# Optimization experiments

Hardware: AMD Instinct MI355X
Metric: run time of the kernel (lower is better)

## Reference

```python
import jax, jax.numpy as jnp
import numpy as np

NUM_HEADS = 16
EMB_SIZE = 1024
HEAD_SIZE = 64


def setup_inputs() -> dict:
    key = jax.random.key(0)
    ks = jax.random.split(key, 9)
    H, E, D = NUM_HEADS, EMB_SIZE, HEAD_SIZE
    s = 1.0 / np.sqrt(E)
    X = jax.random.normal(ks[0], (4, 2048, E), dtype=jnp.float32)
    Wq = jax.random.uniform(ks[1], (H, E, D), jnp.float32, -s, s)
    Wk = jax.random.uniform(ks[2], (H, E, D), jnp.float32, -s, s)
    Wv = jax.random.uniform(ks[3], (H, E, D), jnp.float32, -s, s)
    bq = jax.random.uniform(ks[4], (H, D), jnp.float32, -s, s)
    bk = jax.random.uniform(ks[5], (H, D), jnp.float32, -s, s)
    bv = jax.random.uniform(ks[6], (H, D), jnp.float32, -s, s)
    so = 1.0 / np.sqrt(H * D)
    Wo = jax.random.uniform(ks[7], (H * D, E), jnp.float32, -so, so)
    bo = jax.random.uniform(ks[8], (E,), jnp.float32, -so, so)
    return {"X": X, "Wq": Wq, "Wk": Wk, "Wv": Wv, "bq": bq, "bk": bk, "bv": bv, "Wo": Wo, "bo": bo}


def reference(X, Wq, Wk, Wv, bq, bk, bv, Wo, bo):
    B, S, E = X.shape
    H, _, D = Wq.shape
    # per-head projections (batched over heads)
    q = jnp.einsum('bse,hed->bhsd', X, Wq) + bq[None, :, None, :]
    k = jnp.einsum('bse,hed->bhsd', X, Wk) + bk[None, :, None, :]
    v = jnp.einsum('bse,hed->bhsd', X, Wv) + bv[None, :, None, :]
    # causal scaled-dot-product attention
    scores = jnp.einsum('bhsd,bhtd->bhst', q, k) / jnp.sqrt(jnp.float32(D))
    causal = jnp.tril(jnp.ones((S, S), dtype=bool))
    scores = jnp.where(causal[None, None], scores, jnp.float32(-jnp.inf))
    probs = jax.nn.softmax(scores, axis=-1)
    out = jnp.einsum('bhst,bhtd->bhsd', probs, v)
    # concat heads (head h occupies slots [h*D:(h+1)*D]) then output proj
    concat = out.transpose(0, 2, 1, 3).reshape(B, S, H * D)
    # dropout is identity in eval mode
    return concat @ Wo + bo
```

## Files before the change

### kernel.cpp

```cpp
#include <hip/hip_runtime.h>
#include <stdint.h>


typedef float   f32x4  __attribute__((ext_vector_type(4)));
typedef __bf16  bf16x8 __attribute__((ext_vector_type(8)));
typedef short   short8 __attribute__((ext_vector_type(8)));
typedef unsigned short ushort4v __attribute__((ext_vector_type(4)));

typedef __attribute__((address_space(1))) void GV;
typedef __attribute__((address_space(3))) void LV;

#define DEVI static __device__ __forceinline__

DEVI unsigned short f2bf(float f){
  unsigned u = __float_as_uint(f);
  unsigned r = u + 0x7fffu + ((u>>16)&1u);
  return (unsigned short)(r>>16);
}

DEVI unsigned cvt_pk_bf16(float lo, float hi){
  unsigned r;
  asm("v_cvt_pk_bf16_f32 %0, %1, %2" : "=v"(r) : "v"(lo), "v"(hi));
  return r;
}

DEVI void permlane32_swap(unsigned &a, unsigned &b){
  asm volatile("v_permlane32_swap_b32 %0, %1" : "+v"(a), "+v"(b));
}
DEVI void permlane16_swap(unsigned &a, unsigned &b){
  asm volatile("v_permlane16_swap_b32 %0, %1" : "+v"(a), "+v"(b));
}

DEVI void gl_lds16(const void* g, void* l){
  __builtin_amdgcn_global_load_lds((GV*)g, (LV*)l, 16, 0, 0);
}

#define BAR() asm volatile("s_barrier" ::: "memory")

__global__ __launch_bounds__(256) void pack_x(const float* __restrict__ X,
                                              short* __restrict__ Xb){
  int i = blockIdx.x*256 + threadIdx.x;
  const float4* p = (const float4*)(X + (size_t)i*8);
  float4 a = p[0], b = p[1];
  short8 o;
  o[0]=(short)f2bf(a.x); o[1]=(short)f2bf(a.y); o[2]=(short)f2bf(a.z); o[3]=(short)f2bf(a.w);
  o[4]=(short)f2bf(b.x); o[5]=(short)f2bf(b.y); o[6]=(short)f2bf(b.z); o[7]=(short)f2bf(b.w);
  *(short8*)(Xb + (size_t)i*8) = o;
}

__global__ __launch_bounds__(256) void pack_wqkv(const float* __restrict__ Wq,
                                                 const float* __restrict__ Wk,
                                                 const float* __restrict__ Wv,
                                                 short* __restrict__ Wp){
  int t = blockIdx.x*256 + threadIdx.x;
  int n = t >> 7, kc = t & 127;
  int which = n >> 10, hd = n & 1023, h = hd >> 6, d = hd & 63;
  const float* W = which==0 ? Wq : (which==1 ? Wk : Wv);
  const float* src = W + ((size_t)h*1024 + kc*8)*64 + d;
  short8 o;
  #pragma unroll
  for (int j=0;j<8;++j) o[j] = (short)f2bf(src[(size_t)j*64]);
  *(short8*)(Wp + (size_t)n*1024 + kc*8) = o;
}

__global__ __launch_bounds__(256) void pack_wo(const float* __restrict__ Wo,
                                               short* __restrict__ WoT){
  int t = blockIdx.x*256 + threadIdx.x;
  int n = t >> 7, kc = t & 127;
  const float* src = Wo + (size_t)(kc*8)*1024 + n;
  short8 o;
  #pragma unroll
  for (int j=0;j<8;++j) o[j] = (short)f2bf(src[(size_t)j*1024]);
  *(short8*)(WoT + (size_t)n*1024 + kc*8) = o;
}

__global__ __launch_bounds__(512)
void gemm_qkv(const short* __restrict__ A, const short* __restrict__ Bt,
              const float* __restrict__ b0, const float* __restrict__ b1,
              const float* __restrict__ b2,
              short* __restrict__ Qb, short* __restrict__ Kb, short* __restrict__ Vtb)
{
  __shared__ __align__(16) char sm[2][65536];
  const int K2 = 2048;
  int t = threadIdx.x, lane = t & 63, wid = t >> 6;
  int wr = wid >> 2, wc = wid & 3;
  int l15 = lane & 15, l4 = lane >> 4;
  int swz = (blockIdx.x & 7) * 48 + (blockIdx.x >> 3);
  int bm = swz & 31, bn = swz >> 5;
  size_t abase = (size_t)bm * 256 * K2;
  size_t bbase = (size_t)bn * 256 * K2;

  f32x4 acc[8][4] = {};
  bf16x8 af[8], bfr[4];
  const char* sA; const char* sB;

  auto stageA = [&](int kt, char* buf){
    int kb = kt * 128;
    #pragma unroll
    for (int c = 0; c < 4; ++c){
      int x = c*8192 + t*16;
      int r = x >> 7, z = x & 127;
      int zs = z ^ ((r & 7) << 4);
      gl_lds16((const char*)A + abase + (size_t)r*K2 + kb + zs, buf + c*8192 + wid*1024);
    }
  };
  auto stageB = [&](int kt, char* buf){
    int kb = kt * 128;
    #pragma unroll
    for (int c = 0; c < 4; ++c){
      int x = c*8192 + t*16;
      int r = x >> 7, z = x & 127;
      int zs = z ^ ((r & 7) << 4);
      gl_lds16((const char*)Bt + bbase + (size_t)r*K2 + kb + zs, buf + 32768 + c*8192 + wid*1024);
    }
  };
  auto rd_af = [&](int kk){
    int cb = kk*64 + l4*16;
    #pragma unroll
    for (int i = 0; i < 8; ++i){
      int ra = wr*128 + i*16 + l15;
      af[i] = *(const bf16x8*)(sA + ra*128 + (cb ^ ((ra&7)<<4)));
    }
  };
  auto rd_bf = [&](int kk){
    int cb = kk*64 + l4*16;
    #pragma unroll
    for (int j = 0; j < 4; ++j){
      int rb = wc*64 + j*16 + l15;
      bfr[j] = *(const bf16x8*)(sB + rb*128 + (cb ^ ((rb&7)<<4)));
    }
  };
  auto mm = [&](){
    __builtin_amdgcn_s_setprio(1);
    #pragma unroll
    for (int i = 0; i < 8; ++i)
      #pragma unroll
      for (int j = 0; j < 4; ++j)
        acc[i][j] = __builtin_amdgcn_mfma_f32_16x16x32_bf16(af[i], bfr[j], acc[i][j], 0, 0, 0);
    __builtin_amdgcn_s_setprio(0);
  };

  stageA(0, sm[0]); stageB(0, sm[0]);

  for (int kt = 0; kt < 16; ++kt){
    BAR();
    if (kt < 15){
      char* nb = sm[(kt + 1) & 1];
      stageA(kt + 1, nb); stageB(kt + 1, nb);
      asm volatile("s_waitcnt vmcnt(8)" ::: "memory");
    } else {
      asm volatile("s_waitcnt vmcnt(0)" ::: "memory");
    }
    BAR();
    sA = sm[kt & 1]; sB = sA + 32768;
    rd_af(0); rd_bf(0);
    mm();
    rd_af(1); rd_bf(1);
    mm();
  }

  #pragma unroll
  for (int i = 0; i < 8; ++i){
    int mbase = bm*256 + wr*128 + i*16 + l4*4;
    #pragma unroll
    for (int j = 0; j < 4; ++j){
      int n = bn*256 + wc*64 + j*16 + l15;
      int which = n >> 10, hd = n & 1023, h = hd >> 6, d = hd & 63;
      const float* bp = which==0 ? b0 : (which==1 ? b1 : b2);
      float bias = bp[hd];
      int b = mbase >> 11, sbase = mbase & 2047;
      size_t bh = (size_t)(b*16 + h);
      if (which == 2){
        ushort4v pv;
        #pragma unroll
        for (int r = 0; r < 4; ++r) pv[r] = f2bf(acc[i][j][r] + bias);
        *(ushort4v*)(Vtb + (bh*64 + d)*2048 + sbase) = pv;
      } else {
        short* dst = (which==0 ? Qb : Kb) + bh*2048*64;
        float sc = which==0 ? 0.18033688f : 1.0f;
        #pragma unroll
        for (int r = 0; r < 4; ++r)
          dst[(size_t)(sbase + r)*64 + d] = (short)f2bf((acc[i][j][r] + bias) * sc);
      }
    }
  }
}

__global__ __launch_bounds__(512)
void gemm_out(const short* __restrict__ A, const short* __restrict__ Bt,
              const float* __restrict__ b0, float* __restrict__ Out)
{
  __shared__ __align__(16) char sm[3][49152];
  const int K2 = 2048;
  int t = threadIdx.x, lane = t & 63, wid = t >> 6;
  int wr = wid >> 2, wc = wid & 3;
  int l15 = lane & 15, l4 = lane >> 4;
  int swz = (blockIdx.x & 7) * 32 + (blockIdx.x >> 3);
  int bm = swz & 63, bn = swz >> 6;
  size_t abase = (size_t)bm * 128 * K2;
  size_t bbase = (size_t)bn * 256 * K2;

  f32x4 acc[4][4] = {};
  const char* sA; const char* sB;
  bf16x8 af[4], bfr[4];

  auto stageA = [&](int kt, char* buf){
    int kb = kt * 128;
    #pragma unroll
    for (int c = 0; c < 2; ++c){
      int x = c*8192 + t*16;
      int r = x >> 7, z = x & 127;
      int zs = z ^ ((r & 7) << 4);
      gl_lds16((const char*)A + abase + (size_t)r*K2 + kb + zs, buf + c*8192 + wid*1024);
    }
  };
  auto stageB = [&](int kt, char* buf, int c0){
    int kb = kt * 128;
    #pragma unroll
    for (int c = 0; c < 2; ++c){
      int cc = c0 + c;
      int x = cc*8192 + t*16;
      int r = x >> 7, z = x & 127;
      int zs = z ^ ((r & 7) << 4);
      gl_lds16((const char*)Bt + bbase + (size_t)r*K2 + kb + zs, buf + 16384 + cc*8192 + wid*1024);
    }
  };
  auto rd_af = [&](int kk){
    int cb = kk*64 + l4*16;
    #pragma unroll
    for (int i = 0; i < 4; ++i){
      int ra = wr*64 + i*16 + l15;
      af[i] = *(const bf16x8*)(sA + ra*128 + (cb ^ ((ra&7)<<4)));
    }
  };
  auto rd_bf = [&](int kk, int j0){
    int cb = kk*64 + l4*16;
    #pragma unroll
    for (int j = 0; j < 2; ++j){
      int rb = wc*64 + (j0 + j)*16 + l15;
      bfr[j0 + j] = *(const bf16x8*)(sB + rb*128 + (cb ^ ((rb&7)<<4)));
    }
  };
  auto mm = [&](int j0){
    __builtin_amdgcn_s_setprio(1);
    #pragma unroll
    for (int i = 0; i < 4; ++i)
      #pragma unroll
      for (int j = 0; j < 2; ++j)
        acc[i][j0+j] = __builtin_amdgcn_mfma_f32_16x16x32_bf16(af[i], bfr[j0+j], acc[i][j0+j], 0, 0, 0);
    __builtin_amdgcn_s_setprio(0);
  };

  stageA(0, sm[0]); stageB(0, sm[0], 0); stageB(0, sm[0], 2);
  stageA(1, sm[1]); stageB(1, sm[1], 0); stageB(1, sm[1], 2);

  for (int kt = 0; kt < 16; ++kt){
    if (kt == 15) asm volatile("s_waitcnt vmcnt(0)" ::: "memory");
    else          asm volatile("s_waitcnt vmcnt(6)" ::: "memory");
    BAR();
    sA = sm[kt % 3]; sB = sA + 16384;
    char* nb = sm[(kt + 2) % 3];
    bool st = kt < 14;
    rd_af(0); rd_bf(0, 0);
    if (st) stageA(kt + 2, nb);
    BAR(); mm(0); BAR();
    rd_bf(0, 2);
    if (st) stageB(kt + 2, nb, 0);
    BAR(); mm(2); BAR();
    rd_af(1); rd_bf(1, 0);
    if (st) stageB(kt + 2, nb, 2);
    BAR(); mm(0); BAR();
    rd_bf(1, 2);
    BAR(); mm(2);
  }

  #pragma unroll
  for (int i = 0; i < 4; ++i){
    int mbase = bm*128 + wr*64 + i*16 + l4*4;
    #pragma unroll
    for (int j = 0; j < 4; ++j){
      int n = bn*256 + wc*64 + j*16 + l15;
      float bias = b0[n];
      #pragma unroll
      for (int r = 0; r < 4; ++r)
        Out[(size_t)(mbase + r)*1024 + n] = acc[i][j][r] + bias;
    }
  }
}

__global__ __launch_bounds__(256, 5)
void attn(const short* __restrict__ Qb, const short* __restrict__ Kb,
          const short* __restrict__ Vtb, short* __restrict__ Ob)
{
  __shared__ __align__(16) char smK[2][8192];
  __shared__ __align__(16) char smV[2][8192];
  int t = threadIdx.x, lane = t & 63, wid = t >> 6;
  int l15 = lane & 15, hi = lane >> 4;
  int hi16 = hi*16, hi4 = hi*4;
  int bh = blockIdx.x & 63;
  int qb = 31 - (blockIdx.x >> 6);
  int b = bh >> 4, h = bh & 15;
  int wq0 = qb*64 + wid*16;
  const char* Qh = (const char*)(Qb + (size_t)bh*2048*64);
  const char* Kh = (const char*)(Kb + (size_t)bh*2048*64);
  const char* Vh = (const char*)(Vtb + (size_t)bh*64*2048);

  bf16x8 vones;
  #pragma unroll
  for (int z = 0; z < 8; ++z) vones[z] = (__bf16)1.0f;

  bf16x8 qf[2];
  #pragma unroll
  for (int kk = 0; kk < 2; ++kk)
    qf[kk] = *(const bf16x8*)(Qh + (size_t)(wq0 + l15)*128 + kk*64 + hi16);

  f32x4 oacc[4] = {};
  f32x4 lacc = {};

  int nkt = qb + 1;

  #pragma unroll
  for (int c = 0; c < 2; ++c){
    int x = c*4096 + t*16;
    int r = x >> 7, z = x & 127;
    int zs = z ^ ((r & 7) << 4);
    gl_lds16(Kh + (size_t)r*128 + zs, smK[0] + c*4096 + wid*1024);
    gl_lds16(Vh + (size_t)r*4096 + zs, smV[0] + c*4096 + wid*1024);
  }
  __syncthreads();

  for (int kt = 0; kt < nkt; ++kt){
    int cur = kt & 1;
    if (kt + 1 < nkt){
      int nxt = cur ^ 1;
      #pragma unroll
      for (int c = 0; c < 2; ++c){
        int x = c*4096 + t*16;
        int r = x >> 7, z = x & 127;
        int zs = z ^ ((r & 7) << 4);
        gl_lds16(Kh + (size_t)(kt+1)*8192 + (size_t)r*128 + zs, smK[nxt] + c*4096 + wid*1024);
        gl_lds16(Vh + (size_t)r*4096 + (size_t)(kt+1)*128 + zs, smV[nxt] + c*4096 + wid*1024);
      }
    }
    const char* Kc = smK[cur];
    const char* Vc = smV[cur];
    int kbase = kt * 64;

    f32x4 sa[4];
    __builtin_amdgcn_s_setprio(1);
    #pragma unroll
    for (int nt = 0; nt < 4; ++nt){
      f32x4 a = {};
      #pragma unroll
      for (int kk = 0; kk < 2; ++kk){
        int rk = nt*16 + l15;
        bf16x8 kf = *(const bf16x8*)(Kc + rk*128 + ((kk*64 + hi16) ^ ((rk&7)<<4)));
        a = __builtin_amdgcn_mfma_f32_16x16x32_bf16(kf, qf[kk], a, 0, 0, 0);
      }
      sa[nt] = a;
    }
    __builtin_amdgcn_s_setprio(0);

    if (kt == qb){
      int qrow = wq0 + l15;
      #pragma unroll
      for (int nt = 0; nt < 4; ++nt)
        #pragma unroll
        for (int r = 0; r < 4; ++r)
          if (kbase + nt*16 + hi4 + r > qrow) sa[nt][r] = -1e30f;
    }

    unsigned pw[8];
    #pragma unroll
    for (int nt = 0; nt < 4; ++nt){
      float p0 = exp2f(sa[nt][0]);
      float p1 = exp2f(sa[nt][1]);
      float p2 = exp2f(sa[nt][2]);
      float p3 = exp2f(sa[nt][3]);
      pw[nt*2]   = cvt_pk_bf16(p0, p1);
      pw[nt*2+1] = cvt_pk_bf16(p2, p3);
    }

    union U { unsigned u[4]; bf16x8 v; } f0, f1;
    {
      unsigned a0 = pw[0], b0v = pw[2];
      permlane32_swap(a0, b0v); permlane16_swap(a0, b0v);
      unsigned a1 = pw[1], b1v = pw[3];
      permlane32_swap(a1, b1v); permlane16_swap(a1, b1v);
      f0.u[0] = a0; f0.u[1] = a1; f0.u[2] = b0v; f0.u[3] = b1v;
      unsigned a2 = pw[4], b2v = pw[6];
      permlane32_swap(a2, b2v); permlane16_swap(a2, b2v);
      unsigned a3 = pw[5], b3v = pw[7];
      permlane32_swap(a3, b3v); permlane16_swap(a3, b3v);
      f1.u[0] = a2; f1.u[1] = a3; f1.u[2] = b2v; f1.u[3] = b3v;
    }

    __builtin_amdgcn_s_setprio(1);
    #pragma unroll
    for (int kk = 0; kk < 2; ++kk){
      bf16x8 pf = kk ? f1.v : f0.v;
      lacc = __builtin_amdgcn_mfma_f32_16x16x32_bf16(vones, pf, lacc, 0, 0, 0);
      #pragma unroll
      for (int dt = 0; dt < 4; ++dt){
        int rv = dt*16 + l15;
        bf16x8 vf = *(const bf16x8*)(Vc + rv*128 + ((kk*64 + hi16) ^ ((rv&7)<<4)));
        oacc[dt] = __builtin_amdgcn_mfma_f32_16x16x32_bf16(vf, pf, oacc[dt], 0, 0, 0);
      }
    }
    __builtin_amdgcn_s_setprio(0);

    __syncthreads();
  }

  float inv = 1.0f / lacc[0];
  int srow = wq0 + l15;
  size_t rb = ((size_t)(b*2048 + srow))*1024 + h*64 + hi4;
  #pragma unroll
  for (int dt = 0; dt < 4; ++dt){
    unsigned w0 = cvt_pk_bf16(oacc[dt][0]*inv, oacc[dt][1]*inv);
    unsigned w1 = cvt_pk_bf16(oacc[dt][2]*inv, oacc[dt][3]*inv);
    *(unsigned long long*)(Ob + rb + dt*16) =
        ((unsigned long long)w1 << 32) | (unsigned long long)w0;
  }
}

extern "C" void kernel_launch(void* const* d_in, const int* in_sizes, int n_in,
                              void* d_out, int out_size, void* d_ws, size_t ws_size,
                              hipStream_t stream)
{
  const float* X  = (const float*)d_in[0];
  const float* Wq = (const float*)d_in[1];
  const float* Wk = (const float*)d_in[2];
  const float* Wv = (const float*)d_in[3];
  const float* bq = (const float*)d_in[4];
  const float* bk = (const float*)d_in[5];
  const float* bv = (const float*)d_in[6];
  const float* Wo = (const float*)d_in[7];
  const float* bo = (const float*)d_in[8];
  float* Out = (float*)d_out;

  char* ws = (char*)d_ws;
  short* Xbf  = (short*)(ws);
  short* Wp   = (short*)(ws + 16777216);
  short* WoT  = (short*)(ws + 23068672);
  short* Qb   = (short*)(ws + 25165824);
  short* Kb   = (short*)(ws + 41943040);
  short* Vtb  = (short*)(ws + 58720256);
  short* Ob   = (short*)(ws + 75497472);

  pack_x   <<<4096, 256, 0, stream>>>(X, Xbf);
  pack_wqkv<<<1536, 256, 0, stream>>>(Wq, Wk, Wv, Wp);
  pack_wo  <<< 512, 256, 0, stream>>>(Wo, WoT);

  gemm_qkv<<<384, 512, 0, stream>>>(Xbf, Wp, bq, bk, bv, Qb, Kb, Vtb);
  attn    <<<2048, 256, 0, stream>>>(Qb, Kb, Vtb, Ob);
  gemm_out<<<256, 512, 0, stream>>>(Ob, WoT, bo, Out);
}
```

Baseline: 190.7 us.

## Interleave QKV GEMM global-to-LDS staging with MFMA phases in ping-pong schedule

Restructures the QKV projection GEMM main loop into four sub-phases per k-tile. Each phase reads a slice of A fragments (and all of B up front), issues part of the next tile's global-to-LDS loads, and runs a block of MFMAs bracketed by barriers. The intent is to spread memory issue across the compute, reduce register pressure for A fragments, and keep waves in lockstep so loads and MFMAs overlap better. It adds many more barriers per k-tile, and the partial vmcnt waits need careful ordering to stay correct.

Result: no change. 189.0 us (-0.8%).

```diff
diff --git a/kernel.cpp b/kernel.cpp
--- a/kernel.cpp
+++ b/kernel.cpp
@@ -91,72 +91,83 @@
   size_t bbase = (size_t)bn * 256 * K2;
 
   f32x4 acc[8][4] = {};
-  bf16x8 af[8], bfr[4];
+  bf16x8 af[2][2];
+  bf16x8 bfr[2][4];
   const char* sA; const char* sB;
 
-  auto stageA = [&](int kt, char* buf){
-    int kb = kt * 128;
-    #pragma unroll
-    for (int c = 0; c < 4; ++c){
-      int x = c*8192 + t*16;
-      int r = x >> 7, z = x & 127;
-      int zs = z ^ ((r & 7) << 4);
-      gl_lds16((const char*)A + abase + (size_t)r*K2 + kb + zs, buf + c*8192 + wid*1024);
-    }
-  };
-  auto stageB = [&](int kt, char* buf){
-    int kb = kt * 128;
-    #pragma unroll
-    for (int c = 0; c < 4; ++c){
-      int x = c*8192 + t*16;
-      int r = x >> 7, z = x & 127;
-      int zs = z ^ ((r & 7) << 4);
-      gl_lds16((const char*)Bt + bbase + (size_t)r*K2 + kb + zs, buf + 32768 + c*8192 + wid*1024);
-    }
-  };
-  auto rd_af = [&](int kk){
-    int cb = kk*64 + l4*16;
-    #pragma unroll
-    for (int i = 0; i < 8; ++i){
-      int ra = wr*128 + i*16 + l15;
-      af[i] = *(const bf16x8*)(sA + ra*128 + (cb ^ ((ra&7)<<4)));
-    }
-  };
-  auto rd_bf = [&](int kk){
-    int cb = kk*64 + l4*16;
-    #pragma unroll
-    for (int j = 0; j < 4; ++j){
-      int rb = wc*64 + j*16 + l15;
-      bfr[j] = *(const bf16x8*)(sB + rb*128 + (cb ^ ((rb&7)<<4)));
-    }
-  };
-  auto mm = [&](){
+  int srow8 = t >> 3;
+  int szs0  = (t & 7) * 16;
+  auto stA = [&](int kt, int ca, char* buf){
+    int r = ca*64 + srow8;
+    int zs = szs0 ^ ((r & 7) << 4);
+    gl_lds16((const char*)A + abase + (size_t)r*K2 + kt*128 + zs,
+             buf + ca*8192 + wid*1024);
+  };
+  auto stB = [&](int kt, int cb, char* buf){
+    int r = cb*64 + srow8;
+    int zs = szs0 ^ ((r & 7) << 4);
+    gl_lds16((const char*)Bt + bbase + (size_t)r*K2 + kt*128 + zs,
+             buf + 32768 + cb*8192 + wid*1024);
+  };
+  auto rdA = [&](int p){
+    #pragma unroll
+    for (int kk = 0; kk < 2; ++kk){
+      int cb = kk*64 + l4*16;
+      #pragma unroll
+      for (int u = 0; u < 2; ++u){
+        int ra = wr*128 + (2*p + u)*16 + l15;
+        af[kk][u] = *(const bf16x8*)(sA + ra*128 + (cb ^ ((ra&7)<<4)));
+      }
+    }
+  };
+  auto rdB = [&](){
+    #pragma unroll
+    for (int kk = 0; kk < 2; ++kk){
+      int cb = kk*64 + l4*16;
+      #pragma unroll
+      for (int j = 0; j < 4; ++j){
+        int rb = wc*64 + j*16 + l15;
+        bfr[kk][j] = *(const bf16x8*)(sB + rb*128 + (cb ^ ((rb&7)<<4)));
+      }
+    }
+  };
+  auto mmp = [&](int p){
     __builtin_amdgcn_s_setprio(1);
     #pragma unroll
-    for (int i = 0; i < 8; ++i)
-      #pragma unroll
-      for (int j = 0; j < 4; ++j)
-        acc[i][j] = __builtin_amdgcn_mfma_f32_16x16x32_bf16(af[i], bfr[j], acc[i][j], 0, 0, 0);
+    for (int kk = 0; kk < 2; ++kk)
+      #pragma unroll
+      for (int u = 0; u < 2; ++u)
+        #pragma unroll
+        for (int j = 0; j < 4; ++j)
+          acc[2*p+u][j] = __builtin_amdgcn_mfma_f32_16x16x32_bf16(af[kk][u], bfr[kk][j],
+                                                                  acc[2*p+u][j], 0, 0, 0);
     __builtin_amdgcn_s_setprio(0);
   };
 
-  stageA(0, sm[0]); stageB(0, sm[0]);
+  stB(0,0,sm[0]); stB(0,1,sm[0]); stB(0,2,sm[0]); stB(0,3,sm[0]);
+  stA(0,0,sm[0]); stA(0,2,sm[0]); stA(0,1,sm[0]); stA(0,3,sm[0]);
+  asm volatile("s_waitcnt vmcnt(2)" ::: "memory");
+  BAR();
 
   for (int kt = 0; kt < 16; ++kt){
-    BAR();
-    if (kt < 15){
-      char* nb = sm[(kt + 1) & 1];
-      stageA(kt + 1, nb); stageB(kt + 1, nb);
-      asm volatile("s_waitcnt vmcnt(8)" ::: "memory");
-    } else {
-      asm volatile("s_waitcnt vmcnt(0)" ::: "memory");
-    }
-    BAR();
     sA = sm[kt & 1]; sB = sA + 32768;
-    rd_af(0); rd_bf(0);
-    mm();
-    rd_af(1); rd_bf(1);
-    mm();
+    char* nb = sm[(kt + 1) & 1];
+    bool st = kt < 15;
+    rdB(); rdA(0);
+    if (st){ stB(kt+1, 0, nb); stB(kt+1, 1, nb); }
+    BAR(); mmp(0); BAR();
+    rdA(1);
+    if (st){ stB(kt+1, 2, nb); stB(kt+1, 3, nb);
+             asm volatile("s_waitcnt vmcnt(4)" ::: "memory"); }
+    else   { asm volatile("s_waitcnt vmcnt(0)" ::: "memory"); }
+    BAR(); mmp(1); BAR();
+    rdA(2);
+    if (st){ stA(kt+1, 0, nb); stA(kt+1, 2, nb); }
+    BAR(); mmp(2); BAR();
+    rdA(3);
+    if (st){ stA(kt+1, 1, nb); stA(kt+1, 3, nb);
+             asm volatile("s_waitcnt vmcnt(2)" ::: "memory"); }
+    BAR(); mmp(3); BAR();
   }
 
   #pragma unroll
```

## Merge pack kernels and split QKV GEMM into QK and V launches

Applied to the files above, without the earlier changes.

Fuses the three fp32-to-bf16 pack kernels into a single launch, which saves launch overhead. The single 384-workgroup QKV GEMM becomes two launches. Q/K run on the original 256x256-tile kernel with 256 workgroups. V runs on the 128x256-tile output GEMM kernel, now templated to write the transposed V layout, also with 256 workgroups. The aim is to avoid the 1.5-wave tail of 384 large tiles on the GPU's CUs, at the cost of an extra launch and re-reading X for the V projection.

Measured after the change: 184.0 us (median of 2 runs). 3.5% less time.

```diff
diff --git a/kernel.cpp b/kernel.cpp
--- a/kernel.cpp
+++ b/kernel.cpp
@@ -37,55 +37,54 @@
 
 #define BAR() asm volatile("s_barrier" ::: "memory")
 
-__global__ __launch_bounds__(256) void pack_x(const float* __restrict__ X,
-                                              short* __restrict__ Xb){
-  int i = blockIdx.x*256 + threadIdx.x;
-  const float4* p = (const float4*)(X + (size_t)i*8);
-  float4 a = p[0], b = p[1];
-  short8 o;
-  o[0]=(short)f2bf(a.x); o[1]=(short)f2bf(a.y); o[2]=(short)f2bf(a.z); o[3]=(short)f2bf(a.w);
-  o[4]=(short)f2bf(b.x); o[5]=(short)f2bf(b.y); o[6]=(short)f2bf(b.z); o[7]=(short)f2bf(b.w);
-  *(short8*)(Xb + (size_t)i*8) = o;
-}
-
-__global__ __launch_bounds__(256) void pack_wqkv(const float* __restrict__ Wq,
-                                                 const float* __restrict__ Wk,
-                                                 const float* __restrict__ Wv,
-                                                 short* __restrict__ Wp){
-  int t = blockIdx.x*256 + threadIdx.x;
-  int n = t >> 7, kc = t & 127;
-  int which = n >> 10, hd = n & 1023, h = hd >> 6, d = hd & 63;
-  const float* W = which==0 ? Wq : (which==1 ? Wk : Wv);
-  const float* src = W + ((size_t)h*1024 + kc*8)*64 + d;
-  short8 o;
-  #pragma unroll
-  for (int j=0;j<8;++j) o[j] = (short)f2bf(src[(size_t)j*64]);
-  *(short8*)(Wp + (size_t)n*1024 + kc*8) = o;
-}
-
-__global__ __launch_bounds__(256) void pack_wo(const float* __restrict__ Wo,
-                                               short* __restrict__ WoT){
-  int t = blockIdx.x*256 + threadIdx.x;
-  int n = t >> 7, kc = t & 127;
-  const float* src = Wo + (size_t)(kc*8)*1024 + n;
-  short8 o;
-  #pragma unroll
-  for (int j=0;j<8;++j) o[j] = (short)f2bf(src[(size_t)j*1024]);
-  *(short8*)(WoT + (size_t)n*1024 + kc*8) = o;
+__global__ __launch_bounds__(256)
+void pack_all(const float* __restrict__ X,
+              const float* __restrict__ Wq, const float* __restrict__ Wk,
+              const float* __restrict__ Wv, const float* __restrict__ Wo,
+              short* __restrict__ Xb, short* __restrict__ Wp,
+              short* __restrict__ WoT)
+{
+  int bid = blockIdx.x;
+  if (bid < 4096){
+    int i = bid*256 + threadIdx.x;
+    const float4* p = (const float4*)(X + (size_t)i*8);
+    float4 a = p[0], b = p[1];
+    short8 o;
+    o[0]=(short)f2bf(a.x); o[1]=(short)f2bf(a.y); o[2]=(short)f2bf(a.z); o[3]=(short)f2bf(a.w);
+    o[4]=(short)f2bf(b.x); o[5]=(short)f2bf(b.y); o[6]=(short)f2bf(b.z); o[7]=(short)f2bf(b.w);
+    *(short8*)(Xb + (size_t)i*8) = o;
+  } else if (bid < 5632){
+    int t = (bid - 4096)*256 + threadIdx.x;
+    int n = t >> 7, kc = t & 127;
+    int which = n >> 10, hd = n & 1023, h = hd >> 6, d = hd & 63;
+    const float* W = which==0 ? Wq : (which==1 ? Wk : Wv);
+    const float* src = W + ((size_t)h*1024 + kc*8)*64 + d;
+    short8 o;
+    #pragma unroll
+    for (int j=0;j<8;++j) o[j] = (short)f2bf(src[(size_t)j*64]);
+    *(short8*)(Wp + (size_t)n*1024 + kc*8) = o;
+  } else {
+    int t = (bid - 5632)*256 + threadIdx.x;
+    int n = t >> 7, kc = t & 127;
+    const float* src = Wo + (size_t)(kc*8)*1024 + n;
+    short8 o;
+    #pragma unroll
+    for (int j=0;j<8;++j) o[j] = (short)f2bf(src[(size_t)j*1024]);
+    *(short8*)(WoT + (size_t)n*1024 + kc*8) = o;
+  }
 }
 
 __global__ __launch_bounds__(512)
-void gemm_qkv(const short* __restrict__ A, const short* __restrict__ Bt,
-              const float* __restrict__ b0, const float* __restrict__ b1,
-              const float* __restrict__ b2,
-              short* __restrict__ Qb, short* __restrict__ Kb, short* __restrict__ Vtb)
+void gemm_qk(const short* __restrict__ A, const short* __restrict__ Bt,
+             const float* __restrict__ b0, const float* __restrict__ b1,
+             short* __restrict__ Qb, short* __restrict__ Kb)
 {
   __shared__ __align__(16) char sm[2][65536];
   const int K2 = 2048;
   int t = threadIdx.x, lane = t & 63, wid = t >> 6;
   int wr = wid >> 2, wc = wid & 3;
   int l15 = lane & 15, l4 = lane >> 4;
-  int swz = (blockIdx.x & 7) * 48 + (blockIdx.x >> 3);
+  int swz = (blockIdx.x & 7) * 32 + (blockIdx.x >> 3);
   int bm = swz & 31, bn = swz >> 5;
   size_t abase = (size_t)bm * 256 * K2;
   size_t bbase = (size_t)bn * 256 * K2;
@@ -166,36 +165,31 @@
     for (int j = 0; j < 4; ++j){
       int n = bn*256 + wc*64 + j*16 + l15;
       int which = n >> 10, hd = n & 1023, h = hd >> 6, d = hd & 63;
-      const float* bp = which==0 ? b0 : (which==1 ? b1 : b2);
-      float bias = bp[hd];
+      float bias = (which==0 ? b0 : b1)[hd];
       int b = mbase >> 11, sbase = mbase & 2047;
       size_t bh = (size_t)(b*16 + h);
-      if (which == 2){
-        ushort4v pv;
-        #pragma unroll
-        for (int r = 0; r < 4; ++r) pv[r] = f2bf(acc[i][j][r] + bias);
-        *(ushort4v*)(Vtb + (bh*64 + d)*2048 + sbase) = pv;
-      } else {
-        short* dst = (which==0 ? Qb : Kb) + bh*2048*64;
-        float sc = which==0 ? 0.18033688f : 1.0f;
-        #pragma unroll
-        for (int r = 0; r < 4; ++r)
-          dst[(size_t)(sbase + r)*64 + d] = (short)f2bf((acc[i][j][r] + bias) * sc);
-      }
-    }
-  }
-}
-
+      short* dst = (which==0 ? Qb : Kb) + bh*2048*64;
+      float sc = which==0 ? 0.18033688f : 1.0f;
+      #pragma unroll
+      for (int r = 0; r < 4; ++r)
+        dst[(size_t)(sbase + r)*64 + d] = (short)f2bf((acc[i][j][r] + bias) * sc);
+    }
+  }
+}
+
+template<int MODE>
 __global__ __launch_bounds__(512)
-void gemm_out(const short* __restrict__ A, const short* __restrict__ Bt,
-              const float* __restrict__ b0, float* __restrict__ Out)
+void gemm256(const short* __restrict__ A, const short* __restrict__ Bt,
+             const float* __restrict__ b0,
+             short* __restrict__ Vtb, float* __restrict__ Out)
 {
   __shared__ __align__(16) char sm[3][49152];
   const int K2 = 2048;
   int t = threadIdx.x, lane = t & 63, wid = t >> 6;
   int wr = wid >> 2, wc = wid & 3;
   int l15 = lane & 15, l4 = lane >> 4;
-  int swz = (blockIdx.x & 7) * 32 + (blockIdx.x >> 3);
+  int nwg = gridDim.x, qd = nwg >> 3;
+  int swz = (blockIdx.x & 7) * qd + (blockIdx.x >> 3);
   int bm = swz & 63, bn = swz >> 6;
   size_t abase = (size_t)bm * 128 * K2;
   size_t bbase = (size_t)bn * 256 * K2;
@@ -280,10 +274,21 @@
     #pragma unroll
     for (int j = 0; j < 4; ++j){
       int n = bn*256 + wc*64 + j*16 + l15;
-      float bias = b0[n];
-      #pragma unroll
-      for (int r = 0; r < 4; ++r)
-        Out[(size_t)(mbase + r)*1024 + n] = acc[i][j][r] + bias;
+      if (MODE == 2){
+        int h = n >> 6, d = n & 63;
+        float bias = b0[n];
+        int b = mbase >> 11, sbase = mbase & 2047;
+        size_t bh = (size_t)(b*16 + h);
+        ushort4v pv;
+        #pragma unroll
+        for (int r = 0; r < 4; ++r) pv[r] = f2bf(acc[i][j][r] + bias);
+        *(ushort4v*)(Vtb + (bh*64 + d)*2048 + sbase) = pv;
+      } else {
+        float bias = b0[n];
+        #pragma unroll
+        for (int r = 0; r < 4; ++r)
+          Out[(size_t)(mbase + r)*1024 + n] = acc[i][j][r] + bias;
+      }
     }
   }
 }
@@ -448,11 +453,10 @@
   short* Vtb  = (short*)(ws + 58720256);
   short* Ob   = (short*)(ws + 75497472);
 
-  pack_x   <<<4096, 256, 0, stream>>>(X, Xbf);
-  pack_wqkv<<<1536, 256, 0, stream>>>(Wq, Wk, Wv, Wp);
-  pack_wo  <<< 512, 256, 0, stream>>>(Wo, WoT);
-
-  gemm_qkv<<<384, 512, 0, stream>>>(Xbf, Wp, bq, bk, bv, Qb, Kb, Vtb);
-  attn    <<<2048, 256, 0, stream>>>(Qb, Kb, Vtb, Ob);
-  gemm_out<<<256, 512, 0, stream>>>(Ob, WoT, bo, Out);
-}
+  pack_all<<<6144, 256, 0, stream>>>(X, Wq, Wk, Wv, Wo, Xbf, Wp, WoT);
+
+  gemm_qk   <<<256, 512, 0, stream>>>(Xbf, Wp, bq, bk, Qb, Kb);
+  gemm256<2><<<256, 512, 0, stream>>>(Xbf, Wp + (size_t)2048*1024, bv, Vtb, nullptr);
+  attn      <<<2048, 256, 0, stream>>>(Qb, Kb, Vtb, Ob);
+  gemm256<1><<<256, 512, 0, stream>>>(Ob, WoT, bo, nullptr, Out);
+}
```
